# Optimization experiments

Hardware: AMD Instinct MI355X
Metric: run time of the kernel (lower is better)

## Reference

```python
import jax, jax.numpy as jnp
import numpy as np

B, S_ENC, S_DEC, D_IN, UNITS = 8, 2048, 1024, 512, 512

def setup_inputs() -> dict:
    key = jax.random.key(0)
    k1, k2, k3, k4, k5 = jax.random.split(key, 5)
    scale = 1.0 / np.sqrt(D_IN)
    return {
        "encoding": jax.random.normal(k1, (B, S_ENC, D_IN), dtype=jnp.float32),
        "decoding": jax.random.normal(k2, (B, S_DEC, D_IN), dtype=jnp.float32),
        "Wq": jax.random.normal(k3, (D_IN, UNITS), dtype=jnp.float32) * scale,
        "Wk": jax.random.normal(k4, (D_IN, UNITS), dtype=jnp.float32) * scale,
        "Wv": jax.random.normal(k5, (D_IN, UNITS), dtype=jnp.float32) * scale,
    }

def reference(encoding, decoding, Wq, Wk, Wv):
    # bias-free projections
    q = jnp.einsum('bsd,du->bsu', decoding, Wq)   # [B, S_dec, U]
    k = jnp.einsum('bsd,du->bsu', encoding, Wk)   # [B, S_enc, U]
    v = jnp.einsum('bsd,du->bsu', encoding, Wv)   # [B, S_enc, U]
    # NOTE: original applies no 1/sqrt(d) scaling
    score = jnp.einsum('bqu,bku->bqk', q, k)      # [B, S_dec, S_enc]
    score = jax.nn.softmax(score, axis=2)
    return jnp.einsum('bqk,bku->bqu', score, v)   # [B, S_dec, U]
```

## Files before the change

### kernel.cpp

```cpp
#include <hip/hip_runtime.h>
#include <hip/hip_bf16.h>


typedef __attribute__((ext_vector_type(8))) _Float16 f16x8;
typedef __attribute__((ext_vector_type(4))) _Float16 f16x4;
typedef __attribute__((ext_vector_type(4))) float f32x4;

#define MFMA16(a, b, c) __builtin_amdgcn_mfma_f32_16x16x32_f16(a, b, c, 0, 0, 0)

__device__ __forceinline__ void glds16(const void* g, void* l) {
    __builtin_amdgcn_global_load_lds(
        (const __attribute__((address_space(1))) void*)g,
        (__attribute__((address_space(3))) void*)l, 16, 0, 0);
}

__global__ __launch_bounds__(256) void convert_f16(const float* __restrict__ x,
                                                   _Float16* __restrict__ o) {
    size_t i = ((size_t)blockIdx.x * 256 + threadIdx.x) * 8;
    float4 a0 = *(const float4*)(x + i);
    float4 a1 = *(const float4*)(x + i + 4);
    float v[8] = {a0.x, a0.y, a0.z, a0.w, a1.x, a1.y, a1.z, a1.w};
    f16x8 h;
#pragma unroll
    for (int j = 0; j < 8; ++j) h[j] = (_Float16)v[j];
    *(f16x8*)(o + i) = h;
}

__global__ __launch_bounds__(256) void wtrans_kernel(const float* __restrict__ Wq,
                                                     const float* __restrict__ Wk,
                                                     const float* __restrict__ Wv,
                                                     _Float16* __restrict__ planes) {
    const float* W = blockIdx.z == 0 ? Wq : (blockIdx.z == 1 ? Wk : Wv);
    _Float16* ot = planes + (size_t)blockIdx.z * 262144;
    __shared__ float T[64][65];
    const int d0 = blockIdx.y * 64, u0 = blockIdx.x * 64;
    const int tr = threadIdx.x >> 4, tc = (threadIdx.x & 15) * 4;
#pragma unroll
    for (int j = 0; j < 4; ++j) {
        float4 vv = *(const float4*)(W + (size_t)(d0 + tr + j * 16) * 512 + u0 + tc);
        T[tr + j * 16][tc + 0] = vv.x;
        T[tr + j * 16][tc + 1] = vv.y;
        T[tr + j * 16][tc + 2] = vv.z;
        T[tr + j * 16][tc + 3] = vv.w;
    }
    __syncthreads();
#pragma unroll
    for (int j = 0; j < 4; ++j) {
        int ul = tr + j * 16;
        f16x4 h;
#pragma unroll
        for (int i = 0; i < 4; ++i) h[i] = (_Float16)T[tc + i][ul];
        *(f16x4*)(ot + (size_t)(u0 + ul) * 512 + d0 + tc) = h;
    }
}

template <int BM, int OUT>
__global__ __launch_bounds__(256) void gemm_kernel(
    const _Float16* __restrict__ A, const _Float16* __restrict__ B,
    void* __restrict__ O1,
    int lda, int ldb, int K, int a_row_batch, long b_batch, int ldo) {
    constexpr int BUFSZ = BM * 64 + 8192;
    constexpr int MT = BM / 32;
    constexpr int JA = BM / 64;
    __shared__ __align__(16) char smem[2 * BUFSZ];

    const int tid = threadIdx.x;
    const int wave = tid >> 6, lane = tid & 63;
    const int quad = lane >> 4, m16 = lane & 15;
    const int wr = wave >> 1, wc = wave & 1;
    const int z = blockIdx.z;
    const int row0 = z * a_row_batch + blockIdx.y * BM;
    const int col0 = blockIdx.x * 128;

    const int srowA = wave * (16 * JA) + (lane >> 2);
    const int srowB = wave * 32 + (lane >> 2);
    const int scol = (lane & 3) * 8;
    const _Float16* agp = A + (size_t)(row0 + srowA) * lda + scol;
    const _Float16* bgp = B + (size_t)z * b_batch + (size_t)(col0 + srowB) * ldb + scol;
    const int ldsAoff = wave * (1024 * JA);
    const int ldsBoff = BM * 64 + wave * 2048;

    f32x4 acc[MT][4];
#pragma unroll
    for (int mt = 0; mt < MT; ++mt)
#pragma unroll
        for (int nt = 0; nt < 4; ++nt) acc[mt][nt] = (f32x4){0.f, 0.f, 0.f, 0.f};

    const int nIter = K / 32;
    auto stage = [&](int i, int buf) {
        char* base = smem + buf * BUFSZ;
        const int k0 = i * 32;
#pragma unroll
        for (int j = 0; j < JA; ++j)
            glds16(agp + k0 + j * 16 * lda, base + ldsAoff + j * 1024);
#pragma unroll
        for (int j = 0; j < 2; ++j)
            glds16(bgp + k0 + j * 16 * ldb, base + ldsBoff + j * 1024);
    };

    stage(0, 0);
    for (int i = 0; i < nIter; ++i) {
        __syncthreads();
        if (i + 1 < nIter) stage(i + 1, (i + 1) & 1);
        const char* bb = smem + (i & 1) * BUFSZ;
        const char* pa = bb + (wr * (BM / 2) + m16) * 64 + quad * 16;
        const char* pb = bb + BM * 64 + (wc * 64 + m16) * 64 + quad * 16;
        f16x8 af[MT];
#pragma unroll
        for (int mt = 0; mt < MT; ++mt) af[mt] = *(const f16x8*)(pa + mt * 1024);
#pragma unroll
        for (int nt = 0; nt < 4; ++nt) {
            f16x8 bf = *(const f16x8*)(pb + nt * 1024);
#pragma unroll
            for (int mt = 0; mt < MT; ++mt) acc[mt][nt] = MFMA16(af[mt], bf, acc[mt][nt]);
        }
    }

    if (OUT == 0) {
        _Float16* o = (_Float16*)O1;
#pragma unroll
        for (int mt = 0; mt < MT; ++mt)
#pragma unroll
            for (int nt = 0; nt < 4; ++nt)
#pragma unroll
                for (int rr = 0; rr < 4; ++rr) {
                    int row = row0 + wr * (BM / 2) + mt * 16 + quad * 4 + rr;
                    int col = col0 + wc * 64 + nt * 16 + m16;
                    o[(size_t)row * ldo + col] = (_Float16)acc[mt][nt][rr];
                }
    } else if (OUT == 2) {
        float* o = (float*)O1;
#pragma unroll
        for (int mt = 0; mt < MT; ++mt)
#pragma unroll
            for (int nt = 0; nt < 4; ++nt)
#pragma unroll
                for (int rr = 0; rr < 4; ++rr) {
                    int row = row0 + wr * (BM / 2) + mt * 16 + quad * 4 + rr;
                    int col = col0 + wc * 64 + nt * 16 + m16;
                    o[(size_t)row * ldo + col] = acc[mt][nt][rr];
                }
    } else {
        _Float16* vt = (_Float16*)O1;
        const int row0g = blockIdx.y * 128;
        const int b = row0g >> 11;
        const int s_base = (row0g & 2047) + wr * 64;
        char* reg = smem + wave * 4096;
#pragma unroll
        for (int p = 0; p < 2; ++p) {
            __syncthreads();
#pragma unroll
            for (int nt2 = 0; nt2 < 2; ++nt2) {
                int nt = p * 2 + nt2;
#pragma unroll
                for (int mt = 0; mt < 4; ++mt) {
                    f16x4 pk;
#pragma unroll
                    for (int rr = 0; rr < 4; ++rr) pk[rr] = (_Float16)acc[mt][nt][rr];
                    *(f16x4*)(reg + (nt2 * 16 + m16) * 128 + (mt * 16 + quad * 4) * 2) = pk;
                }
            }
            __syncthreads();
            const int u_base = col0 + wc * 64 + p * 32;
#pragma unroll
            for (int j = 0; j < 4; ++j) {
                int n = j * 8 + (lane >> 3);
                int mo = (lane & 7) * 8;
                f16x8 val = *(const f16x8*)(reg + n * 128 + mo * 2);
                *(f16x8*)(vt + (size_t)(b * 512 + u_base + n) * 2048 + s_base + mo) = val;
            }
        }
    }
}

__global__ __launch_bounds__(256) void softmax_kernel(const float* __restrict__ S,
                                                      _Float16* __restrict__ P) {
    const int row = blockIdx.x;
    const int tid = threadIdx.x;
    const int wave = tid >> 6, lane = tid & 63;
    __shared__ float red[8];

    const float* sp = S + (size_t)row * 2048 + tid * 8;
    float4 x0 = *(const float4*)sp;
    float4 x1 = *(const float4*)(sp + 4);
    float v[8] = {x0.x, x0.y, x0.z, x0.w, x1.x, x1.y, x1.z, x1.w};

    float mx = v[0];
#pragma unroll
    for (int i = 1; i < 8; ++i) mx = fmaxf(mx, v[i]);
#pragma unroll
    for (int off = 32; off > 0; off >>= 1) mx = fmaxf(mx, __shfl_down(mx, off));
    if (lane == 0) red[wave] = mx;
    __syncthreads();
    if (tid == 0) red[4] = fmaxf(fmaxf(red[0], red[1]), fmaxf(red[2], red[3]));
    __syncthreads();
    mx = red[4];

    float e[8];
    float sum = 0.f;
#pragma unroll
    for (int i = 0; i < 8; ++i) {
        e[i] = exp2f((v[i] - mx) * 1.44269504088896f);
        sum += e[i];
    }
#pragma unroll
    for (int off = 32; off > 0; off >>= 1) sum += __shfl_down(sum, off);
    if (lane == 0) red[wave] = sum;
    __syncthreads();
    if (tid == 0) red[5] = red[0] + red[1] + red[2] + red[3];
    __syncthreads();
    float inv = 1.0f / red[5];

    f16x8 ov;
#pragma unroll
    for (int i = 0; i < 8; ++i) ov[i] = (_Float16)(e[i] * inv);
    *(f16x8*)(P + (size_t)row * 2048 + tid * 8) = ov;
}

extern "C" void kernel_launch(void* const* d_in, const int* in_sizes, int n_in,
                              void* d_out, int out_size, void* d_ws, size_t ws_size,
                              hipStream_t stream) {
    const float* enc = (const float*)d_in[0];
    const float* dec = (const float*)d_in[1];
    const float* Wq = (const float*)d_in[2];
    const float* Wk = (const float*)d_in[3];
    const float* Wv = (const float*)d_in[4];
    float* out = (float*)d_out;

    char* ws = (char*)d_ws;
    _Float16* qh = (_Float16*)(ws);
    _Float16* kh = (_Float16*)(ws + ((size_t)8 << 20));
    _Float16* P = (_Float16*)(ws);
    _Float16* vt = (_Float16*)(ws + ((size_t)32 << 20));
    float* S = (float*)(ws + ((size_t)48 << 20));
    _Float16* dech = (_Float16*)(ws + ((size_t)48 << 20));
    _Float16* wts = (_Float16*)(ws + ((size_t)56 << 20));
    _Float16* ench = (_Float16*)(ws + ((size_t)112 << 20));

    dim3 blk(256);
    convert_f16<<<4096, blk, 0, stream>>>(enc, ench);
    convert_f16<<<2048, blk, 0, stream>>>(dec, dech);
    wtrans_kernel<<<dim3(8, 8, 3), blk, 0, stream>>>(Wq, Wk, Wv, wts);
    gemm_kernel<64, 0><<<dim3(4, 128, 1), blk, 0, stream>>>(
        dech, wts, qh, 512, 512, 512, 0, 0, 512);
    gemm_kernel<128, 0><<<dim3(4, 128, 1), blk, 0, stream>>>(
        ench, wts + 262144, kh, 512, 512, 512, 0, 0, 512);
    gemm_kernel<128, 1><<<dim3(4, 128, 1), blk, 0, stream>>>(
        ench, wts + 524288, vt, 512, 512, 512, 0, 0, 0);
    gemm_kernel<128, 2><<<dim3(16, 8, 8), blk, 0, stream>>>(
        qh, kh, S, 512, 512, 512, 1024, (long)2048 * 512, 2048);
    softmax_kernel<<<8192, blk, 0, stream>>>(S, P);
    gemm_kernel<64, 2><<<dim3(4, 16, 8), blk, 0, stream>>>(
        P, vt, out, 2048, 2048, 2048, 1024, (long)512 * 2048, 512);
}
```

Baseline: 233.1 us.

## Fuse QK^T, softmax and PV into a single flash-attention kernel

Replaces the separate score GEMM, softmax kernel and PV GEMM with one online-softmax attention kernel. Each block keeps 32 query rows in LDS, streams K chunks through double-buffered LDS, keeps running max and sum, and pipelines the PV of the previous chunk with the QK of the current one. This removes the round trips of the fp32 score matrix and the f16 probability matrix through global memory. In exchange only 256 blocks are launched, there are many barriers per chunk, and V is read directly from global memory without LDS staging.

```diff
diff --git a/kernel.cpp b/kernel.cpp
--- a/kernel.cpp
+++ b/kernel.cpp
@@ -7,12 +7,194 @@
 typedef __attribute__((ext_vector_type(4))) float f32x4;
 
 #define MFMA16(a, b, c) __builtin_amdgcn_mfma_f32_16x16x32_f16(a, b, c, 0, 0, 0)
+#define L2E 1.44269504088896f
 
 __device__ __forceinline__ void glds16(const void* g, void* l) {
     __builtin_amdgcn_global_load_lds(
         (const __attribute__((address_space(1))) void*)g,
         (__attribute__((address_space(3))) void*)l, 16, 0, 0);
 }
+
+#define QS_OFF 0
+#define KS_OFF 32768
+#define PS_OFF 65536
+#define MS_OFF 70144
+#define CHMAX_OFF 70400
+#define CHSUM_OFF 71424
+#define SMEM_SZ 72448
+
+__global__ __launch_bounds__(512, 4) void attn_kernel(
+    const _Float16* __restrict__ qh, const _Float16* __restrict__ kh,
+    const _Float16* __restrict__ vt, float* __restrict__ out) {
+    __shared__ __align__(16) char smem[SMEM_SZ];
+    const int tid = threadIdx.x;
+    const int wave = tid >> 6, lane = tid & 63;
+    const int quad = lane >> 4, m16 = lane & 15;
+    const int qg = wave & 1, kg = wave >> 1;
+    const int uw = wave * 64;
+    const int z = blockIdx.x & 7;
+    const int qt = blockIdx.x >> 3;
+    const int g0 = z * 1024 + qt * 32;
+
+    {
+        const int r8w = wave;
+#pragma unroll
+        for (int r = 0; r < 4; ++r)
+            glds16(qh + (size_t)(g0 + r * 8 + wave) * 512 + (lane ^ r8w) * 8,
+                   smem + QS_OFF + r * 8192 + wave * 1024);
+    }
+    if (tid < 32) *(float*)(smem + MS_OFF + tid * 4) = -1e30f;
+
+    const int krl = tid >> 4;
+    const _Float16* khp = kh + (size_t)(z * 2048 + krl) * 512 + (m16 ^ (krl & 7)) * 8;
+    auto stageK = [&](int tt2) {
+        const int ci2 = tt2 >> 2, ds2 = tt2 & 3, buf2 = tt2 & 1;
+#pragma unroll
+        for (int r = 0; r < 2; ++r)
+            glds16(khp + ci2 * 32768 + r * 16384 + ds2 * 128,
+                   smem + KS_OFF + buf2 * 16384 + r * 8192 + wave * 1024);
+    };
+    stageK(0);
+
+    f32x4 O[2][4];
+#pragma unroll
+    for (int mt = 0; mt < 2; ++mt)
+#pragma unroll
+        for (int nt = 0; nt < 4; ++nt) O[mt][nt] = (f32x4){0.f, 0.f, 0.f, 0.f};
+    float l_[2][4] = {{0.f, 0.f, 0.f, 0.f}, {0.f, 0.f, 0.f, 0.f}};
+    f32x4 sacc;
+
+    const int sw = m16 & 7;
+    const int qrow_base = QS_OFF + (qg * 16 + m16) * 1024;
+    const int krow_base = KS_OFF + (kg * 16 + m16) * 256;
+    const _Float16* vbase = vt + (size_t)(z * 512 + uw + m16) * 2048 + quad * 8;
+
+    auto S_sub = [&](int buf, int sub) {
+#pragma unroll
+        for (int ks = 0; ks < 4; ++ks) {
+            f16x8 af = *(const f16x8*)(smem + qrow_base +
+                                       (((sub * 16 + ks * 4 + quad) ^ sw) << 4));
+            f16x8 bf = *(const f16x8*)(smem + krow_base + buf * 16384 +
+                                       (((ks * 4 + quad) ^ sw) << 4));
+            sacc = MFMA16(af, bf, sacc);
+        }
+    };
+    auto PV_piece = [&](int cip, int nt) {
+#pragma unroll
+        for (int kk = 0; kk < 2; ++kk) {
+            f16x8 vf = *(const f16x8*)(vbase + (size_t)nt * 16 * 2048 + cip * 64 + kk * 32);
+#pragma unroll
+            for (int mt = 0; mt < 2; ++mt) {
+                f16x8 pf = *(const f16x8*)(smem + PS_OFF + (mt * 16 + m16) * 144 +
+                                           kk * 64 + quad * 16);
+                O[mt][nt] = MFMA16(pf, vf, O[mt][nt]);
+            }
+        }
+    };
+    auto segment = [&](int cip) {
+        const int b = cip & 1;
+        const int row = lane & 31;
+        float cm = *(const float*)(smem + CHMAX_OFF + b * 512 + row * 4);
+#pragma unroll
+        for (int k2 = 1; k2 < 4; ++k2)
+            cm = fmaxf(cm, *(const float*)(smem + CHMAX_OFF + b * 512 + k2 * 128 + row * 4));
+        float mo = *(const float*)(smem + MS_OFF + b * 128 + row * 4);
+        float mn = fmaxf(mo, cm);
+        float al = exp2f((mo - mn) * L2E);
+        if (wave == 0 && lane < 32) *(float*)(smem + MS_OFF + (b ^ 1) * 128 + row * 4) = mn;
+        float p[4];
+#pragma unroll
+        for (int r = 0; r < 4; ++r) {
+            float mnr = __shfl(mn, qg * 16 + quad * 4 + r);
+            p[r] = exp2f((sacc[r] - mnr) * L2E);
+            *(_Float16*)(smem + PS_OFF + (qg * 16 + quad * 4 + r) * 144 +
+                         (kg * 16 + m16) * 2) = (_Float16)p[r];
+        }
+        float ps[4] = {p[0], p[1], p[2], p[3]};
+#pragma unroll
+        for (int mask = 1; mask < 16; mask <<= 1)
+#pragma unroll
+            for (int r = 0; r < 4; ++r) ps[r] += __shfl_xor(ps[r], mask);
+        if (m16 == 0) {
+#pragma unroll
+            for (int r = 0; r < 4; ++r)
+                *(float*)(smem + CHSUM_OFF + b * 512 + kg * 128 +
+                          (qg * 16 + quad * 4 + r) * 4) = ps[r];
+        }
+#pragma unroll
+        for (int mt = 0; mt < 2; ++mt)
+#pragma unroll
+            for (int rr = 0; rr < 4; ++rr) {
+                float a2 = __shfl(al, mt * 16 + quad * 4 + rr);
+#pragma unroll
+                for (int nt = 0; nt < 4; ++nt) O[mt][nt][rr] *= a2;
+            }
+    };
+    auto l_update = [&](int cip) {
+        const int b = cip & 1;
+        const int row = lane & 31;
+        float cs = *(const float*)(smem + CHSUM_OFF + b * 512 + row * 4);
+#pragma unroll
+        for (int k2 = 1; k2 < 4; ++k2)
+            cs += *(const float*)(smem + CHSUM_OFF + b * 512 + k2 * 128 + row * 4);
+        float alo = exp2f((*(const float*)(smem + MS_OFF + b * 128 + row * 4) -
+                           *(const float*)(smem + MS_OFF + (b ^ 1) * 128 + row * 4)) * L2E);
+#pragma unroll
+        for (int mt = 0; mt < 2; ++mt)
+#pragma unroll
+            for (int rr = 0; rr < 4; ++rr) {
+                int orow = mt * 16 + quad * 4 + rr;
+                l_[mt][rr] = l_[mt][rr] * __shfl(alo, orow) + __shfl(cs, orow);
+            }
+    };
+
+    for (int ci = 0; ci < 32; ++ci) {
+        __syncthreads();
+        if (ci > 0) segment(ci - 1);
+        __syncthreads();
+        if (ci > 0) l_update(ci - 1);
+        sacc = (f32x4){0.f, 0.f, 0.f, 0.f};
+        stageK(4 * ci + 1);
+        S_sub(0 , 0);
+        if (ci > 0) PV_piece(ci - 1, 0);
+#pragma unroll
+        for (int sub = 1; sub < 4; ++sub) {
+            const int tt = 4 * ci + sub;
+            __syncthreads();
+            if (tt + 1 < 128) stageK(tt + 1);
+            S_sub(tt & 1, sub);
+            if (ci > 0) PV_piece(ci - 1, sub);
+        }
+        f32x4 tm = sacc;
+#pragma unroll
+        for (int mask = 1; mask < 16; mask <<= 1)
+#pragma unroll
+            for (int r = 0; r < 4; ++r) tm[r] = fmaxf(tm[r], __shfl_xor(tm[r], mask));
+        if (m16 == 0) {
+#pragma unroll
+            for (int r = 0; r < 4; ++r)
+                *(float*)(smem + CHMAX_OFF + (ci & 1) * 512 + kg * 128 +
+                          (qg * 16 + quad * 4 + r) * 4) = tm[r];
+        }
+    }
+    __syncthreads();
+    segment(31);
+    __syncthreads();
+    l_update(31);
+#pragma unroll
+    for (int nt = 0; nt < 4; ++nt) PV_piece(31, nt);
+#pragma unroll
+    for (int mt = 0; mt < 2; ++mt)
+#pragma unroll
+        for (int rr = 0; rr < 4; ++rr) {
+            float linv = 1.0f / l_[mt][rr];
+            int grow = g0 + mt * 16 + quad * 4 + rr;
+#pragma unroll
+            for (int nt = 0; nt < 4; ++nt)
+                out[(size_t)grow * 512 + uw + nt * 16 + m16] = O[mt][nt][rr] * linv;
+        }
+}
+
 
 __global__ __launch_bounds__(256) void convert_f16(const float* __restrict__ x,
                                                    _Float16* __restrict__ o) {
@@ -128,20 +310,8 @@
                     int col = col0 + wc * 64 + nt * 16 + m16;
                     o[(size_t)row * ldo + col] = (_Float16)acc[mt][nt][rr];
                 }
-    } else if (OUT == 2) {
-        float* o = (float*)O1;
-#pragma unroll
-        for (int mt = 0; mt < MT; ++mt)
-#pragma unroll
-            for (int nt = 0; nt < 4; ++nt)
-#pragma unroll
-                for (int rr = 0; rr < 4; ++rr) {
-                    int row = row0 + wr * (BM / 2) + mt * 16 + quad * 4 + rr;
-                    int col = col0 + wc * 64 + nt * 16 + m16;
-                    o[(size_t)row * ldo + col] = acc[mt][nt][rr];
-                }
     } else {
-        _Float16* vt = (_Float16*)O1;
+        _Float16* vtp = (_Float16*)O1;
         const int row0g = blockIdx.y * 128;
         const int b = row0g >> 11;
         const int s_base = (row0g & 2047) + wr * 64;
@@ -167,54 +337,10 @@
                 int n = j * 8 + (lane >> 3);
                 int mo = (lane & 7) * 8;
                 f16x8 val = *(const f16x8*)(reg + n * 128 + mo * 2);
-                *(f16x8*)(vt + (size_t)(b * 512 + u_base + n) * 2048 + s_base + mo) = val;
-            }
-        }
-    }
-}
-
-__global__ __launch_bounds__(256) void softmax_kernel(const float* __restrict__ S,
-                                                      _Float16* __restrict__ P) {
-    const int row = blockIdx.x;
-    const int tid = threadIdx.x;
-    const int wave = tid >> 6, lane = tid & 63;
-    __shared__ float red[8];
-
-    const float* sp = S + (size_t)row * 2048 + tid * 8;
-    float4 x0 = *(const float4*)sp;
-    float4 x1 = *(const float4*)(sp + 4);
-    float v[8] = {x0.x, x0.y, x0.z, x0.w, x1.x, x1.y, x1.z, x1.w};
-
-    float mx = v[0];
-#pragma unroll
-    for (int i = 1; i < 8; ++i) mx = fmaxf(mx, v[i]);
-#pragma unroll
-    for (int off = 32; off > 0; off >>= 1) mx = fmaxf(mx, __shfl_down(mx, off));
-    if (lane == 0) red[wave] = mx;
-    __syncthreads();
-    if (tid == 0) red[4] = fmaxf(fmaxf(red[0], red[1]), fmaxf(red[2], red[3]));
-    __syncthreads();
-    mx = red[4];
-
-    float e[8];
-    float sum = 0.f;
-#pragma unroll
-    for (int i = 0; i < 8; ++i) {
-        e[i] = exp2f((v[i] - mx) * 1.44269504088896f);
-        sum += e[i];
-    }
-#pragma unroll
-    for (int off = 32; off > 0; off >>= 1) sum += __shfl_down(sum, off);
-    if (lane == 0) red[wave] = sum;
-    __syncthreads();
-    if (tid == 0) red[5] = red[0] + red[1] + red[2] + red[3];
-    __syncthreads();
-    float inv = 1.0f / red[5];
-
-    f16x8 ov;
-#pragma unroll
-    for (int i = 0; i < 8; ++i) ov[i] = (_Float16)(e[i] * inv);
-    *(f16x8*)(P + (size_t)row * 2048 + tid * 8) = ov;
+                *(f16x8*)(vtp + (size_t)(b * 512 + u_base + n) * 2048 + s_base + mo) = val;
+            }
+        }
+    }
 }
 
 extern "C" void kernel_launch(void* const* d_in, const int* in_sizes, int n_in,
@@ -230,9 +356,7 @@
     char* ws = (char*)d_ws;
     _Float16* qh = (_Float16*)(ws);
     _Float16* kh = (_Float16*)(ws + ((size_t)8 << 20));
-    _Float16* P = (_Float16*)(ws);
     _Float16* vt = (_Float16*)(ws + ((size_t)32 << 20));
-    float* S = (float*)(ws + ((size_t)48 << 20));
     _Float16* dech = (_Float16*)(ws + ((size_t)48 << 20));
     _Float16* wts = (_Float16*)(ws + ((size_t)56 << 20));
     _Float16* ench = (_Float16*)(ws + ((size_t)112 << 20));
@@ -247,9 +371,5 @@
         ench, wts + 262144, kh, 512, 512, 512, 0, 0, 512);
     gemm_kernel<128, 1><<<dim3(4, 128, 1), blk, 0, stream>>>(
         ench, wts + 524288, vt, 512, 512, 512, 0, 0, 0);
-    gemm_kernel<128, 2><<<dim3(16, 8, 8), blk, 0, stream>>>(
-        qh, kh, S, 512, 512, 512, 1024, (long)2048 * 512, 2048);
-    softmax_kernel<<<8192, blk, 0, stream>>>(S, P);
-    gemm_kernel<64, 2><<<dim3(4, 16, 8), blk, 0, stream>>>(
-        P, vt, out, 2048, 2048, 2048, 1024, (long)512 * 2048, 512);
-}
+    attn_kernel<<<256, 512, 0, stream>>>(qh, kh, vt, out);
+}
```

Result: slower. 375.0 us (+60.9%).
